# Kernel tuning notes

Measured on AMD Instinct MI355X. Metric: run time of the kernel, lower is better.

Reference implementation:

```python
import jax, jax.numpy as jnp
import numpy as np


def setup_inputs() -> dict:
    key = jax.random.key(0)
    ks = jax.random.split(key, 8)
    B, CAST, H, IN = 2048, 128, 256, 256
    return {
        "x": jax.random.normal(ks[0], (B, IN), dtype=jnp.float32),
        "batch_idxs": jnp.arange(B, dtype=jnp.int64),
        "actor_ids": jax.random.randint(ks[1], (B,), 0, CAST).astype(jnp.int64),
        "story_stop_idxs": jax.random.randint(ks[2], (128,), 0, B).astype(jnp.int64),
        "state": jax.random.normal(ks[3], (B, CAST, H), dtype=jnp.float32),
        "w_ih": jax.random.normal(ks[4], (3 * H, IN), dtype=jnp.float32) * 0.05,
        "w_hh": jax.random.normal(ks[5], (3 * H, H), dtype=jnp.float32) * 0.05,
        "b_ih": jax.random.normal(ks[6], (3 * H,), dtype=jnp.float32) * 0.05,
        "b_hh": jax.random.normal(ks[7], (3 * H,), dtype=jnp.float32) * 0.05,
    }


def _gru_cell(x, h, w_ih, w_hh, b_ih, b_hh):
    # torch.nn.GRUCell math
    H = h.shape[-1]
    gi = x @ w_ih.T + b_ih  # [n, 3H]
    gh = h @ w_hh.T + b_hh  # [n, 3H]
    i_r, i_z, i_n = gi[:, :H], gi[:, H:2 * H], gi[:, 2 * H:]
    h_r, h_z, h_n = gh[:, :H], gh[:, H:2 * H], gh[:, 2 * H:]
    r = jax.nn.sigmoid(i_r + h_r)
    z = jax.nn.sigmoid(i_z + h_z)
    n = jnp.tanh(i_n + r * h_n)
    return (1.0 - z) * n + z * h


def reference(x, batch_idxs, actor_ids, story_stop_idxs, state, w_ih, w_hh, b_ih, b_hh):
    cast_size = state.shape[1]
    actor_ids = jnp.clip(actor_ids, 0, cast_size - 1)
    aid = actor_ids[batch_idxs]  # convert_idxs: actor slot per active story
    # gather indexed actor states
    selected = state[batch_idxs, aid]  # [n_active, H]
    # GRU-cell update
    new_selected = _gru_cell(x, selected, w_ih, w_hh, b_ih, b_hh)
    # scatter back into persistent memory
    new_state = state.at[batch_idxs, aid].set(new_selected)
    # zero out finished stories
    new_state = new_state.at[story_stop_idxs].set(0.0)
    return new_selected, new_state
```

## Files before the change

kernel.cpp:

```cpp
#include <hip/hip_runtime.h>

#define B_TOTAL 2048
#define CAST    128
#define HDIM    256
#define INDIM   256
#define BM      8
#define GRU_BLOCKS (B_TOTAL / BM)
#define ROW_F4     (CAST * HDIM / 4)

typedef float fx4 __attribute__((ext_vector_type(4)));

__global__ __launch_bounds__(256) void k_init(int* rowaid, int* rowstop) {
    int t = blockIdx.x * blockDim.x + threadIdx.x;
    if (t < B_TOTAL) { rowaid[t] = -1; rowstop[t] = 0; }
}

__global__ __launch_bounds__(256) void k_prep(
    const int* __restrict__ batch_idxs, const int* __restrict__ actor_ids,
    const int* __restrict__ story_stop, int n_stop,
    const float* __restrict__ w_ih, const float* __restrict__ w_hh,
    int* rowaid, int* rowstop, float* wtI, float* wtH) {
    const int h = threadIdx.x;
    if (blockIdx.x < 8) {
        int t = blockIdx.x * 256 + h;
        int row = batch_idxs[t];
        int a = actor_ids[row];
        a = a < 0 ? 0 : (a > CAST - 1 ? CAST - 1 : a);
        rowaid[row] = a;
        if (t < n_stop) rowstop[story_stop[t]] = 1;
    } else {
        int id  = blockIdx.x - 8;
        int mat = id / 192;
        int rem = id % 192;
        int g   = rem / 64;
        int k4  = rem % 64;
        const float* w = mat ? w_hh : w_ih;
        float*      wt = mat ? wtH  : wtI;
        float4 wv = *(const float4*)(w + ((size_t)(g * HDIM + h) * INDIM + k4 * 4));
        *(float4*)(wt + ((size_t)((k4 * 3 + g) * HDIM + h)) * 4) = wv;
    }
}

__global__ __launch_bounds__(256) void k_main(
    const float* __restrict__ x, const int* __restrict__ batch_idxs,
    const int* __restrict__ actor_ids, const float* __restrict__ state,
    const float* __restrict__ wtI, const float* __restrict__ wtH,
    const float* __restrict__ b_ih, const float* __restrict__ b_hh,
    const int* __restrict__ rowaid, const int* __restrict__ rowstop,
    float* __restrict__ out_sel, float* __restrict__ out_state) {
    __shared__ float xs[BM][INDIM];
    __shared__ float ss[BM][HDIM];
    const int h = threadIdx.x;

    if (blockIdx.x < GRU_BLOCKS) {
        const int b0 = blockIdx.x * BM;
        #pragma unroll
        for (int r = 0; r < BM; ++r) {
            int g  = b0 + r;
            int bi = batch_idxs[g];
            int a  = actor_ids[bi];
            a = a < 0 ? 0 : (a > CAST - 1 ? CAST - 1 : a);
            xs[r][h] = x[(size_t)g * INDIM + h];
            ss[r][h] = state[((size_t)bi * CAST + a) * HDIM + h];
        }
        __syncthreads();

        float air[BM], aiz[BM], ain[BM], ahr[BM], ahz[BM], ahn[BM];
        #pragma unroll
        for (int r = 0; r < BM; ++r) { air[r]=0.f; aiz[r]=0.f; ain[r]=0.f; ahr[r]=0.f; ahz[r]=0.f; ahn[r]=0.f; }

        const float4* __restrict__ wtI4 = (const float4*)wtI;
        const float4* __restrict__ wtH4 = (const float4*)wtH;

        for (int k4 = 0; k4 < INDIM / 4; ++k4) {
            float4 wir = wtI4[(k4 * 3 + 0) * HDIM + h];
            float4 wiz = wtI4[(k4 * 3 + 1) * HDIM + h];
            float4 win = wtI4[(k4 * 3 + 2) * HDIM + h];
            float4 whr = wtH4[(k4 * 3 + 0) * HDIM + h];
            float4 whz = wtH4[(k4 * 3 + 1) * HDIM + h];
            float4 whn = wtH4[(k4 * 3 + 2) * HDIM + h];
            #pragma unroll
            for (int r = 0; r < BM; ++r) {
                float4 xv = *(const float4*)(&xs[r][k4 * 4]);
                float4 sv = *(const float4*)(&ss[r][k4 * 4]);
                air[r] = fmaf(xv.w, wir.w, fmaf(xv.z, wir.z, fmaf(xv.y, wir.y, fmaf(xv.x, wir.x, air[r]))));
                aiz[r] = fmaf(xv.w, wiz.w, fmaf(xv.z, wiz.z, fmaf(xv.y, wiz.y, fmaf(xv.x, wiz.x, aiz[r]))));
                ain[r] = fmaf(xv.w, win.w, fmaf(xv.z, win.z, fmaf(xv.y, win.y, fmaf(xv.x, win.x, ain[r]))));
                ahr[r] = fmaf(sv.w, whr.w, fmaf(sv.z, whr.z, fmaf(sv.y, whr.y, fmaf(sv.x, whr.x, ahr[r]))));
                ahz[r] = fmaf(sv.w, whz.w, fmaf(sv.z, whz.z, fmaf(sv.y, whz.y, fmaf(sv.x, whz.x, ahz[r]))));
                ahn[r] = fmaf(sv.w, whn.w, fmaf(sv.z, whn.z, fmaf(sv.y, whn.y, fmaf(sv.x, whn.x, ahn[r]))));
            }
        }

        const float bir = b_ih[h], biz = b_ih[HDIM + h], bin = b_ih[2 * HDIM + h];
        const float bhr = b_hh[h], bhz = b_hh[HDIM + h], bhn = b_hh[2 * HDIM + h];

        #pragma unroll
        for (int r = 0; r < BM; ++r) {
            int g  = b0 + r;
            int bi = batch_idxs[g];
            int a  = actor_ids[bi];
            a = a < 0 ? 0 : (a > CAST - 1 ? CAST - 1 : a);
            float ir = air[r] + bir, iz = aiz[r] + biz, inn = ain[r] + bin;
            float hr = ahr[r] + bhr, hz = ahz[r] + bhz, hn = ahn[r] + bhn;
            float rr = 1.f / (1.f + __expf(-(ir + hr)));
            float zz = 1.f / (1.f + __expf(-(iz + hz)));
            float nn = tanhf(inn + rr * hn);
            float val = (1.f - zz) * nn + zz * ss[r][h];
            out_sel[(size_t)g * HDIM + h] = val;
            if (!rowstop[bi]) out_state[((size_t)bi * CAST + a) * HDIM + h] = val;
        }
    } else {
        const int  b = blockIdx.x - GRU_BLOCKS;
        const int  t = threadIdx.x;
        const long base = (long)b * ROW_F4;
        const fx4* __restrict__ src = (const fx4*)state + base + t;
        fx4* __restrict__ dst = (fx4*)out_state + base + t;

        if (rowstop[b]) {
            const fx4 z = (fx4)(0.f);
            #pragma unroll
            for (int j = 0; j < ROW_F4 / 256; ++j)
                __builtin_nontemporal_store(z, dst + j * 256);
            return;
        }

        const int aid = __builtin_amdgcn_readfirstlane(rowaid[b]);
        const int w   = __builtin_amdgcn_readfirstlane(t >> 6);
        const int jskip = ((aid & 3) == w) ? (aid >> 2) : -1;

        #pragma unroll
        for (int g2 = 0; g2 < 2; ++g2) {
            fx4 d[16];
            #pragma unroll
            for (int i = 0; i < 16; ++i)
                d[i] = __builtin_nontemporal_load(src + (g2 * 16 + i) * 256);
            #pragma unroll
            for (int i = 0; i < 16; ++i) {
                if (g2 * 16 + i != jskip)
                    __builtin_nontemporal_store(d[i], dst + (g2 * 16 + i) * 256);
            }
        }
    }
}

extern "C" void kernel_launch(void* const* d_in, const int* in_sizes, int n_in,
                              void* d_out, int out_size, void* d_ws, size_t ws_size,
                              hipStream_t stream) {
    const float* x          = (const float*)d_in[0];
    const int*   batch_idxs = (const int*)d_in[1];
    const int*   actor_ids  = (const int*)d_in[2];
    const int*   story_stop = (const int*)d_in[3];
    const float* state      = (const float*)d_in[4];
    const float* w_ih       = (const float*)d_in[5];
    const float* w_hh       = (const float*)d_in[6];
    const float* b_ih       = (const float*)d_in[7];
    const float* b_hh       = (const float*)d_in[8];
    const int    n_stop     = in_sizes[3];

    float* out_sel   = (float*)d_out;
    float* out_state = out_sel + (size_t)B_TOTAL * HDIM;

    int*   rowaid  = (int*)d_ws;
    int*   rowstop = rowaid + B_TOTAL;
    float* wtI     = (float*)((char*)d_ws + 16384);
    float* wtH     = wtI + (size_t)3 * HDIM * INDIM;

    k_init<<<(B_TOTAL + 255) / 256, 256, 0, stream>>>(rowaid, rowstop);
    k_prep<<<8 + 384, 256, 0, stream>>>(batch_idxs, actor_ids, story_stop, n_stop,
                                        w_ih, w_hh, rowaid, rowstop, wtI, wtH);
    k_main<<<GRU_BLOCKS + B_TOTAL, 256, 0, stream>>>(
        x, batch_idxs, actor_ids, state, wtI, wtH, b_ih, b_hh,
        rowaid, rowstop, out_sel, out_state);
}
```

Before: 159.8 us.

## Move bulk state copy into prep kernel and scatter GRU results afterward

The full state copy now runs in the prep kernel as a grid-strided, coalesced copy alongside the weight transpose. The GRU kernel then overwrites the selected rows and zeroes the stopped rows, so the copy no longer needs per-row actor-skip logic or the rowaid table. The init kernel becomes a memset. In exchange the copy writes every selected slot and the GRU kernel writes them again. The zeroing blocks and the GRU writes also run concurrently, and correctness depends on the rowstop check preventing a race on the same rows.

```diff
diff --git a/kernel.cpp b/kernel.cpp
--- a/kernel.cpp
+++ b/kernel.cpp
@@ -7,140 +7,127 @@
 #define BM      8
 #define GRU_BLOCKS (B_TOTAL / BM)
 #define ROW_F4     (CAST * HDIM / 4)
+#define COPY_BLOCKS 2048
+#define N4_TOTAL   ((long)B_TOTAL * CAST * HDIM / 4)
 
 typedef float fx4 __attribute__((ext_vector_type(4)));
 
-__global__ __launch_bounds__(256) void k_init(int* rowaid, int* rowstop) {
-    int t = blockIdx.x * blockDim.x + threadIdx.x;
-    if (t < B_TOTAL) { rowaid[t] = -1; rowstop[t] = 0; }
-}
-
-__global__ __launch_bounds__(256) void k_prep(
-    const int* __restrict__ batch_idxs, const int* __restrict__ actor_ids,
+__global__ __launch_bounds__(256) void k_copyprep(
+    const float* __restrict__ state, float* __restrict__ out_state,
     const int* __restrict__ story_stop, int n_stop,
     const float* __restrict__ w_ih, const float* __restrict__ w_hh,
-    int* rowaid, int* rowstop, float* wtI, float* wtH) {
-    const int h = threadIdx.x;
-    if (blockIdx.x < 8) {
-        int t = blockIdx.x * 256 + h;
-        int row = batch_idxs[t];
-        int a = actor_ids[row];
-        a = a < 0 ? 0 : (a > CAST - 1 ? CAST - 1 : a);
-        rowaid[row] = a;
+    int* rowstop, float* wtI, float* wtH) {
+    const int t = threadIdx.x;
+    if (blockIdx.x < COPY_BLOCKS) {
+        const long stride = (long)COPY_BLOCKS * 256;
+        const long base = (long)blockIdx.x * 256 + t;
+        const fx4* __restrict__ src = (const fx4*)state;
+        fx4* __restrict__ dst = (fx4*)out_state;
+        #pragma unroll
+        for (int g = 0; g < 4; ++g) {
+            fx4 d[8];
+            #pragma unroll
+            for (int i = 0; i < 8; ++i)
+                d[i] = src[base + (long)(g * 8 + i) * stride];
+            #pragma unroll
+            for (int i = 0; i < 8; ++i)
+                __builtin_nontemporal_store(d[i], &dst[base + (long)(g * 8 + i) * stride]);
+        }
+    } else if (blockIdx.x == COPY_BLOCKS) {
         if (t < n_stop) rowstop[story_stop[t]] = 1;
     } else {
-        int id  = blockIdx.x - 8;
+        int id  = blockIdx.x - (COPY_BLOCKS + 1);
         int mat = id / 192;
         int rem = id % 192;
         int g   = rem / 64;
         int k4  = rem % 64;
         const float* w = mat ? w_hh : w_ih;
         float*      wt = mat ? wtH  : wtI;
-        float4 wv = *(const float4*)(w + ((size_t)(g * HDIM + h) * INDIM + k4 * 4));
-        *(float4*)(wt + ((size_t)((k4 * 3 + g) * HDIM + h)) * 4) = wv;
+        float4 wv = *(const float4*)(w + ((size_t)(g * HDIM + t) * INDIM + k4 * 4));
+        *(float4*)(wt + ((size_t)((k4 * 3 + g) * HDIM + t)) * 4) = wv;
     }
 }
 
-__global__ __launch_bounds__(256) void k_main(
+__global__ __launch_bounds__(256) void k_gru(
     const float* __restrict__ x, const int* __restrict__ batch_idxs,
     const int* __restrict__ actor_ids, const float* __restrict__ state,
     const float* __restrict__ wtI, const float* __restrict__ wtH,
     const float* __restrict__ b_ih, const float* __restrict__ b_hh,
-    const int* __restrict__ rowaid, const int* __restrict__ rowstop,
-    float* __restrict__ out_sel, float* __restrict__ out_state) {
+    const int* __restrict__ rowstop, const int* __restrict__ story_stop,
+    int n_stop, float* __restrict__ out_sel, float* __restrict__ out_state) {
     __shared__ float xs[BM][INDIM];
     __shared__ float ss[BM][HDIM];
     const int h = threadIdx.x;
 
-    if (blockIdx.x < GRU_BLOCKS) {
-        const int b0 = blockIdx.x * BM;
-        #pragma unroll
-        for (int r = 0; r < BM; ++r) {
-            int g  = b0 + r;
-            int bi = batch_idxs[g];
-            int a  = actor_ids[bi];
-            a = a < 0 ? 0 : (a > CAST - 1 ? CAST - 1 : a);
-            xs[r][h] = x[(size_t)g * INDIM + h];
-            ss[r][h] = state[((size_t)bi * CAST + a) * HDIM + h];
-        }
-        __syncthreads();
-
-        float air[BM], aiz[BM], ain[BM], ahr[BM], ahz[BM], ahn[BM];
-        #pragma unroll
-        for (int r = 0; r < BM; ++r) { air[r]=0.f; aiz[r]=0.f; ain[r]=0.f; ahr[r]=0.f; ahz[r]=0.f; ahn[r]=0.f; }
-
-        const float4* __restrict__ wtI4 = (const float4*)wtI;
-        const float4* __restrict__ wtH4 = (const float4*)wtH;
-
-        for (int k4 = 0; k4 < INDIM / 4; ++k4) {
-            float4 wir = wtI4[(k4 * 3 + 0) * HDIM + h];
-            float4 wiz = wtI4[(k4 * 3 + 1) * HDIM + h];
-            float4 win = wtI4[(k4 * 3 + 2) * HDIM + h];
-            float4 whr = wtH4[(k4 * 3 + 0) * HDIM + h];
-            float4 whz = wtH4[(k4 * 3 + 1) * HDIM + h];
-            float4 whn = wtH4[(k4 * 3 + 2) * HDIM + h];
-            #pragma unroll
-            for (int r = 0; r < BM; ++r) {
-                float4 xv = *(const float4*)(&xs[r][k4 * 4]);
-                float4 sv = *(const float4*)(&ss[r][k4 * 4]);
-                air[r] = fmaf(xv.w, wir.w, fmaf(xv.z, wir.z, fmaf(xv.y, wir.y, fmaf(xv.x, wir.x, air[r]))));
-                aiz[r] = fmaf(xv.w, wiz.w, fmaf(xv.z, wiz.z, fmaf(xv.y, wiz.y, fmaf(xv.x, wiz.x, aiz[r]))));
-                ain[r] = fmaf(xv.w, win.w, fmaf(xv.z, win.z, fmaf(xv.y, win.y, fmaf(xv.x, win.x, ain[r]))));
-                ahr[r] = fmaf(sv.w, whr.w, fmaf(sv.z, whr.z, fmaf(sv.y, whr.y, fmaf(sv.x, whr.x, ahr[r]))));
-                ahz[r] = fmaf(sv.w, whz.w, fmaf(sv.z, whz.z, fmaf(sv.y, whz.y, fmaf(sv.x, whz.x, ahz[r]))));
-                ahn[r] = fmaf(sv.w, whn.w, fmaf(sv.z, whn.z, fmaf(sv.y, whn.y, fmaf(sv.x, whn.x, ahn[r]))));
-            }
-        }
-
-        const float bir = b_ih[h], biz = b_ih[HDIM + h], bin = b_ih[2 * HDIM + h];
-        const float bhr = b_hh[h], bhz = b_hh[HDIM + h], bhn = b_hh[2 * HDIM + h];
-
-        #pragma unroll
-        for (int r = 0; r < BM; ++r) {
-            int g  = b0 + r;
-            int bi = batch_idxs[g];
-            int a  = actor_ids[bi];
-            a = a < 0 ? 0 : (a > CAST - 1 ? CAST - 1 : a);
-            float ir = air[r] + bir, iz = aiz[r] + biz, inn = ain[r] + bin;
-            float hr = ahr[r] + bhr, hz = ahz[r] + bhz, hn = ahn[r] + bhn;
-            float rr = 1.f / (1.f + __expf(-(ir + hr)));
-            float zz = 1.f / (1.f + __expf(-(iz + hz)));
-            float nn = tanhf(inn + rr * hn);
-            float val = (1.f - zz) * nn + zz * ss[r][h];
-            out_sel[(size_t)g * HDIM + h] = val;
-            if (!rowstop[bi]) out_state[((size_t)bi * CAST + a) * HDIM + h] = val;
-        }
-    } else {
-        const int  b = blockIdx.x - GRU_BLOCKS;
-        const int  t = threadIdx.x;
-        const long base = (long)b * ROW_F4;
-        const fx4* __restrict__ src = (const fx4*)state + base + t;
-        fx4* __restrict__ dst = (fx4*)out_state + base + t;
-
-        if (rowstop[b]) {
+    if (blockIdx.x >= GRU_BLOCKS) {
+        int zb = blockIdx.x - GRU_BLOCKS;
+        if (zb < n_stop) {
+            long base = (long)story_stop[zb] * ROW_F4;
+            fx4* __restrict__ dst = (fx4*)out_state + base + h;
             const fx4 z = (fx4)(0.f);
             #pragma unroll
             for (int j = 0; j < ROW_F4 / 256; ++j)
                 __builtin_nontemporal_store(z, dst + j * 256);
-            return;
         }
+        return;
+    }
 
-        const int aid = __builtin_amdgcn_readfirstlane(rowaid[b]);
-        const int w   = __builtin_amdgcn_readfirstlane(t >> 6);
-        const int jskip = ((aid & 3) == w) ? (aid >> 2) : -1;
+    const int b0 = blockIdx.x * BM;
+    #pragma unroll
+    for (int r = 0; r < BM; ++r) {
+        int g  = b0 + r;
+        int bi = batch_idxs[g];
+        int a  = actor_ids[bi];
+        a = a < 0 ? 0 : (a > CAST - 1 ? CAST - 1 : a);
+        xs[r][h] = x[(size_t)g * INDIM + h];
+        ss[r][h] = state[((size_t)bi * CAST + a) * HDIM + h];
+    }
+    __syncthreads();
 
+    float air[BM], aiz[BM], ain[BM], ahr[BM], ahz[BM], ahn[BM];
+    #pragma unroll
+    for (int r = 0; r < BM; ++r) { air[r]=0.f; aiz[r]=0.f; ain[r]=0.f; ahr[r]=0.f; ahz[r]=0.f; ahn[r]=0.f; }
+
+    const float4* __restrict__ wtI4 = (const float4*)wtI;
+    const float4* __restrict__ wtH4 = (const float4*)wtH;
+
+    for (int k4 = 0; k4 < INDIM / 4; ++k4) {
+        float4 wir = wtI4[(k4 * 3 + 0) * HDIM + h];
+        float4 wiz = wtI4[(k4 * 3 + 1) * HDIM + h];
+        float4 win = wtI4[(k4 * 3 + 2) * HDIM + h];
+        float4 whr = wtH4[(k4 * 3 + 0) * HDIM + h];
+        float4 whz = wtH4[(k4 * 3 + 1) * HDIM + h];
+        float4 whn = wtH4[(k4 * 3 + 2) * HDIM + h];
         #pragma unroll
-        for (int g2 = 0; g2 < 2; ++g2) {
-            fx4 d[16];
-            #pragma unroll
-            for (int i = 0; i < 16; ++i)
-                d[i] = __builtin_nontemporal_load(src + (g2 * 16 + i) * 256);
-            #pragma unroll
-            for (int i = 0; i < 16; ++i) {
-                if (g2 * 16 + i != jskip)
-                    __builtin_nontemporal_store(d[i], dst + (g2 * 16 + i) * 256);
-            }
+        for (int r = 0; r < BM; ++r) {
+            float4 xv = *(const float4*)(&xs[r][k4 * 4]);
+            float4 sv = *(const float4*)(&ss[r][k4 * 4]);
+            air[r] = fmaf(xv.w, wir.w, fmaf(xv.z, wir.z, fmaf(xv.y, wir.y, fmaf(xv.x, wir.x, air[r]))));
+            aiz[r] = fmaf(xv.w, wiz.w, fmaf(xv.z, wiz.z, fmaf(xv.y, wiz.y, fmaf(xv.x, wiz.x, aiz[r]))));
+            ain[r] = fmaf(xv.w, win.w, fmaf(xv.z, win.z, fmaf(xv.y, win.y, fmaf(xv.x, win.x, ain[r]))));
+            ahr[r] = fmaf(sv.w, whr.w, fmaf(sv.z, whr.z, fmaf(sv.y, whr.y, fmaf(sv.x, whr.x, ahr[r]))));
+            ahz[r] = fmaf(sv.w, whz.w, fmaf(sv.z, whz.z, fmaf(sv.y, whz.y, fmaf(sv.x, whz.x, ahz[r]))));
+            ahn[r] = fmaf(sv.w, whn.w, fmaf(sv.z, whn.z, fmaf(sv.y, whn.y, fmaf(sv.x, whn.x, ahn[r]))));
         }
+    }
+
+    const float bir = b_ih[h], biz = b_ih[HDIM + h], bin = b_ih[2 * HDIM + h];
+    const float bhr = b_hh[h], bhz = b_hh[HDIM + h], bhn = b_hh[2 * HDIM + h];
+
+    #pragma unroll
+    for (int r = 0; r < BM; ++r) {
+        int g  = b0 + r;
+        int bi = batch_idxs[g];
+        int a  = actor_ids[bi];
+        a = a < 0 ? 0 : (a > CAST - 1 ? CAST - 1 : a);
+        float ir = air[r] + bir, iz = aiz[r] + biz, inn = ain[r] + bin;
+        float hr = ahr[r] + bhr, hz = ahz[r] + bhz, hn = ahn[r] + bhn;
+        float rr = 1.f / (1.f + __expf(-(ir + hr)));
+        float zz = 1.f / (1.f + __expf(-(iz + hz)));
+        float nn = tanhf(inn + rr * hn);
+        float val = (1.f - zz) * nn + zz * ss[r][h];
+        out_sel[(size_t)g * HDIM + h] = val;
+        if (!rowstop[bi]) out_state[((size_t)bi * CAST + a) * HDIM + h] = val;
     }
 }
 
@@ -161,15 +148,14 @@
     float* out_sel   = (float*)d_out;
     float* out_state = out_sel + (size_t)B_TOTAL * HDIM;
 
-    int*   rowaid  = (int*)d_ws;
-    int*   rowstop = rowaid + B_TOTAL;
+    int*   rowstop = (int*)d_ws;
     float* wtI     = (float*)((char*)d_ws + 16384);
     float* wtH     = wtI + (size_t)3 * HDIM * INDIM;
 
-    k_init<<<(B_TOTAL + 255) / 256, 256, 0, stream>>>(rowaid, rowstop);
-    k_prep<<<8 + 384, 256, 0, stream>>>(batch_idxs, actor_ids, story_stop, n_stop,
-                                        w_ih, w_hh, rowaid, rowstop, wtI, wtH);
-    k_main<<<GRU_BLOCKS + B_TOTAL, 256, 0, stream>>>(
+    hipMemsetAsync(rowstop, 0, B_TOTAL * sizeof(int), stream);
+    k_copyprep<<<COPY_BLOCKS + 1 + 384, 256, 0, stream>>>(
+        state, out_state, story_stop, n_stop, w_ih, w_hh, rowstop, wtI, wtH);
+    k_gru<<<GRU_BLOCKS + 128, 256, 0, stream>>>(
         x, batch_idxs, actor_ids, state, wtI, wtH, b_ih, b_hh,
-        rowaid, rowstop, out_sel, out_state);
+        rowstop, story_stop, n_stop, out_sel, out_state);
 }
```

Result: slower. 200.2 us (+25.3%).

## Stream state copy through LDS with global_load_lds and reorder copy/GRU blocks

Applied to the files above, without the earlier changes.

The bulk state copy now issues direct global-to-LDS loads in batches of eight 16-byte loads, then reads back from LDS and stores to global. Each wave now owns a contiguous quarter of a row instead of striding across it. Copy blocks are scheduled before the GRU blocks, and the init kernel is replaced by two hipMemsetAsync calls. The aim is higher copy bandwidth and less launch overhead. In exchange, shared memory per block rises to 32 KB, which can lower occupancy, and the copy drops its nontemporal hints, waits on vmcnt(0) every batch, and keeps fewer loads in flight per thread.

```diff
diff --git a/kernel.cpp b/kernel.cpp
--- a/kernel.cpp
+++ b/kernel.cpp
@@ -5,14 +5,16 @@
 #define HDIM    256
 #define INDIM   256
 #define BM      8
-#define GRU_BLOCKS (B_TOTAL / BM)
-#define ROW_F4     (CAST * HDIM / 4)
+#define GRU_BLOCKS  (B_TOTAL / BM)
+#define COPY_BLOCKS B_TOTAL
+#define ROW_FLOATS  (CAST * HDIM)
 
 typedef float fx4 __attribute__((ext_vector_type(4)));
 
-__global__ __launch_bounds__(256) void k_init(int* rowaid, int* rowstop) {
-    int t = blockIdx.x * blockDim.x + threadIdx.x;
-    if (t < B_TOTAL) { rowaid[t] = -1; rowstop[t] = 0; }
+__device__ __forceinline__ void gld_lds16(const float* g, float* l) {
+    __builtin_amdgcn_global_load_lds(
+        (const __attribute__((address_space(1))) void*)g,
+        (__attribute__((address_space(3))) void*)l, 16, 0, 0);
 }
 
 __global__ __launch_bounds__(256) void k_prep(
@@ -20,14 +22,14 @@
     const int* __restrict__ story_stop, int n_stop,
     const float* __restrict__ w_ih, const float* __restrict__ w_hh,
     int* rowaid, int* rowstop, float* wtI, float* wtH) {
-    const int h = threadIdx.x;
+    const int t = threadIdx.x;
     if (blockIdx.x < 8) {
-        int t = blockIdx.x * 256 + h;
-        int row = batch_idxs[t];
+        int g = blockIdx.x * 256 + t;
+        int row = batch_idxs[g];
         int a = actor_ids[row];
         a = a < 0 ? 0 : (a > CAST - 1 ? CAST - 1 : a);
         rowaid[row] = a;
-        if (t < n_stop) rowstop[story_stop[t]] = 1;
+        if (g < n_stop) rowstop[story_stop[g]] = 1;
     } else {
         int id  = blockIdx.x - 8;
         int mat = id / 192;
@@ -36,8 +38,8 @@
         int k4  = rem % 64;
         const float* w = mat ? w_hh : w_ih;
         float*      wt = mat ? wtH  : wtI;
-        float4 wv = *(const float4*)(w + ((size_t)(g * HDIM + h) * INDIM + k4 * 4));
-        *(float4*)(wt + ((size_t)((k4 * 3 + g) * HDIM + h)) * 4) = wv;
+        float4 wv = *(const float4*)(w + ((size_t)(g * HDIM + t) * INDIM + k4 * 4));
+        *(float4*)(wt + ((size_t)((k4 * 3 + g) * HDIM + t)) * 4) = wv;
     }
 }
 
@@ -48,99 +50,107 @@
     const float* __restrict__ b_ih, const float* __restrict__ b_hh,
     const int* __restrict__ rowaid, const int* __restrict__ rowstop,
     float* __restrict__ out_sel, float* __restrict__ out_state) {
-    __shared__ float xs[BM][INDIM];
-    __shared__ float ss[BM][HDIM];
+    __shared__ float smem[8192];
     const int h = threadIdx.x;
 
-    if (blockIdx.x < GRU_BLOCKS) {
-        const int b0 = blockIdx.x * BM;
-        #pragma unroll
-        for (int r = 0; r < BM; ++r) {
-            int g  = b0 + r;
-            int bi = batch_idxs[g];
-            int a  = actor_ids[bi];
-            a = a < 0 ? 0 : (a > CAST - 1 ? CAST - 1 : a);
-            xs[r][h] = x[(size_t)g * INDIM + h];
-            ss[r][h] = state[((size_t)bi * CAST + a) * HDIM + h];
-        }
-        __syncthreads();
-
-        float air[BM], aiz[BM], ain[BM], ahr[BM], ahz[BM], ahn[BM];
-        #pragma unroll
-        for (int r = 0; r < BM; ++r) { air[r]=0.f; aiz[r]=0.f; ain[r]=0.f; ahr[r]=0.f; ahz[r]=0.f; ahn[r]=0.f; }
-
-        const float4* __restrict__ wtI4 = (const float4*)wtI;
-        const float4* __restrict__ wtH4 = (const float4*)wtH;
-
-        for (int k4 = 0; k4 < INDIM / 4; ++k4) {
-            float4 wir = wtI4[(k4 * 3 + 0) * HDIM + h];
-            float4 wiz = wtI4[(k4 * 3 + 1) * HDIM + h];
-            float4 win = wtI4[(k4 * 3 + 2) * HDIM + h];
-            float4 whr = wtH4[(k4 * 3 + 0) * HDIM + h];
-            float4 whz = wtH4[(k4 * 3 + 1) * HDIM + h];
-            float4 whn = wtH4[(k4 * 3 + 2) * HDIM + h];
-            #pragma unroll
-            for (int r = 0; r < BM; ++r) {
-                float4 xv = *(const float4*)(&xs[r][k4 * 4]);
-                float4 sv = *(const float4*)(&ss[r][k4 * 4]);
-                air[r] = fmaf(xv.w, wir.w, fmaf(xv.z, wir.z, fmaf(xv.y, wir.y, fmaf(xv.x, wir.x, air[r]))));
-                aiz[r] = fmaf(xv.w, wiz.w, fmaf(xv.z, wiz.z, fmaf(xv.y, wiz.y, fmaf(xv.x, wiz.x, aiz[r]))));
-                ain[r] = fmaf(xv.w, win.w, fmaf(xv.z, win.z, fmaf(xv.y, win.y, fmaf(xv.x, win.x, ain[r]))));
-                ahr[r] = fmaf(sv.w, whr.w, fmaf(sv.z, whr.z, fmaf(sv.y, whr.y, fmaf(sv.x, whr.x, ahr[r]))));
-                ahz[r] = fmaf(sv.w, whz.w, fmaf(sv.z, whz.z, fmaf(sv.y, whz.y, fmaf(sv.x, whz.x, ahz[r]))));
-                ahn[r] = fmaf(sv.w, whn.w, fmaf(sv.z, whn.z, fmaf(sv.y, whn.y, fmaf(sv.x, whn.x, ahn[r]))));
-            }
-        }
-
-        const float bir = b_ih[h], biz = b_ih[HDIM + h], bin = b_ih[2 * HDIM + h];
-        const float bhr = b_hh[h], bhz = b_hh[HDIM + h], bhn = b_hh[2 * HDIM + h];
-
-        #pragma unroll
-        for (int r = 0; r < BM; ++r) {
-            int g  = b0 + r;
-            int bi = batch_idxs[g];
-            int a  = actor_ids[bi];
-            a = a < 0 ? 0 : (a > CAST - 1 ? CAST - 1 : a);
-            float ir = air[r] + bir, iz = aiz[r] + biz, inn = ain[r] + bin;
-            float hr = ahr[r] + bhr, hz = ahz[r] + bhz, hn = ahn[r] + bhn;
-            float rr = 1.f / (1.f + __expf(-(ir + hr)));
-            float zz = 1.f / (1.f + __expf(-(iz + hz)));
-            float nn = tanhf(inn + rr * hn);
-            float val = (1.f - zz) * nn + zz * ss[r][h];
-            out_sel[(size_t)g * HDIM + h] = val;
-            if (!rowstop[bi]) out_state[((size_t)bi * CAST + a) * HDIM + h] = val;
-        }
-    } else {
-        const int  b = blockIdx.x - GRU_BLOCKS;
-        const int  t = threadIdx.x;
-        const long base = (long)b * ROW_F4;
-        const fx4* __restrict__ src = (const fx4*)state + base + t;
-        fx4* __restrict__ dst = (fx4*)out_state + base + t;
+    if (blockIdx.x < COPY_BLOCKS) {
+        const int  b    = blockIdx.x;
+        const int  w    = h >> 6;
+        const int  lane = h & 63;
+        const long qbase = (long)b * ROW_FLOATS + (long)w * 8192;
+        float* __restrict__ dst = out_state + qbase + lane * 4;
 
         if (rowstop[b]) {
             const fx4 z = (fx4)(0.f);
             #pragma unroll
-            for (int j = 0; j < ROW_F4 / 256; ++j)
-                __builtin_nontemporal_store(z, dst + j * 256);
+            for (int op = 0; op < 32; ++op)
+                __builtin_nontemporal_store(z, (fx4*)(dst + op * 256));
             return;
         }
 
+        const float* __restrict__ src = state + qbase + lane * 4;
+        float* lw = smem + w * 2048;
         const int aid = __builtin_amdgcn_readfirstlane(rowaid[b]);
-        const int w   = __builtin_amdgcn_readfirstlane(t >> 6);
-        const int jskip = ((aid & 3) == w) ? (aid >> 2) : -1;
+        const int sk  = aid - w * 32;
 
         #pragma unroll
-        for (int g2 = 0; g2 < 2; ++g2) {
-            fx4 d[16];
+        for (int bt = 0; bt < 4; ++bt) {
             #pragma unroll
-            for (int i = 0; i < 16; ++i)
-                d[i] = __builtin_nontemporal_load(src + (g2 * 16 + i) * 256);
+            for (int k = 0; k < 8; ++k)
+                gld_lds16(src + (bt * 8 + k) * 256, lw + k * 256);
+            asm volatile("s_waitcnt vmcnt(0)" ::: "memory");
+            __builtin_amdgcn_sched_barrier(0);
             #pragma unroll
-            for (int i = 0; i < 16; ++i) {
-                if (g2 * 16 + i != jskip)
-                    __builtin_nontemporal_store(d[i], dst + (g2 * 16 + i) * 256);
+            for (int k = 0; k < 8; ++k) {
+                const int op = bt * 8 + k;
+                if (op != sk) {
+                    fx4 v = *(const fx4*)(lw + k * 256 + lane * 4);
+                    *(fx4*)(dst + op * 256) = v;
+                }
             }
         }
+        return;
+    }
+
+    float (*xs)[INDIM] = (float(*)[INDIM])smem;
+    float (*ss)[HDIM]  = (float(*)[HDIM])(smem + BM * INDIM);
+    const int b0 = (blockIdx.x - COPY_BLOCKS) * BM;
+
+    #pragma unroll
+    for (int r = 0; r < BM; ++r) {
+        int g  = b0 + r;
+        int bi = batch_idxs[g];
+        int a  = actor_ids[bi];
+        a = a < 0 ? 0 : (a > CAST - 1 ? CAST - 1 : a);
+        xs[r][h] = x[(size_t)g * INDIM + h];
+        ss[r][h] = state[((size_t)bi * CAST + a) * HDIM + h];
+    }
+    __syncthreads();
+
+    float air[BM], aiz[BM], ain[BM], ahr[BM], ahz[BM], ahn[BM];
+    #pragma unroll
+    for (int r = 0; r < BM; ++r) { air[r]=0.f; aiz[r]=0.f; ain[r]=0.f; ahr[r]=0.f; ahz[r]=0.f; ahn[r]=0.f; }
+
+    const float4* __restrict__ wtI4 = (const float4*)wtI;
+    const float4* __restrict__ wtH4 = (const float4*)wtH;
+
+    for (int k4 = 0; k4 < INDIM / 4; ++k4) {
+        float4 wir = wtI4[(k4 * 3 + 0) * HDIM + h];
+        float4 wiz = wtI4[(k4 * 3 + 1) * HDIM + h];
+        float4 win = wtI4[(k4 * 3 + 2) * HDIM + h];
+        float4 whr = wtH4[(k4 * 3 + 0) * HDIM + h];
+        float4 whz = wtH4[(k4 * 3 + 1) * HDIM + h];
+        float4 whn = wtH4[(k4 * 3 + 2) * HDIM + h];
+        #pragma unroll
+        for (int r = 0; r < BM; ++r) {
+            float4 xv = *(const float4*)(&xs[r][k4 * 4]);
+            float4 sv = *(const float4*)(&ss[r][k4 * 4]);
+            air[r] = fmaf(xv.w, wir.w, fmaf(xv.z, wir.z, fmaf(xv.y, wir.y, fmaf(xv.x, wir.x, air[r]))));
+            aiz[r] = fmaf(xv.w, wiz.w, fmaf(xv.z, wiz.z, fmaf(xv.y, wiz.y, fmaf(xv.x, wiz.x, aiz[r]))));
+            ain[r] = fmaf(xv.w, win.w, fmaf(xv.z, win.z, fmaf(xv.y, win.y, fmaf(xv.x, win.x, ain[r]))));
+            ahr[r] = fmaf(sv.w, whr.w, fmaf(sv.z, whr.z, fmaf(sv.y, whr.y, fmaf(sv.x, whr.x, ahr[r]))));
+            ahz[r] = fmaf(sv.w, whz.w, fmaf(sv.z, whz.z, fmaf(sv.y, whz.y, fmaf(sv.x, whz.x, ahz[r]))));
+            ahn[r] = fmaf(sv.w, whn.w, fmaf(sv.z, whn.z, fmaf(sv.y, whn.y, fmaf(sv.x, whn.x, ahn[r]))));
+        }
+    }
+
+    const float bir = b_ih[h], biz = b_ih[HDIM + h], bin = b_ih[2 * HDIM + h];
+    const float bhr = b_hh[h], bhz = b_hh[HDIM + h], bhn = b_hh[2 * HDIM + h];
+
+    #pragma unroll
+    for (int r = 0; r < BM; ++r) {
+        int g  = b0 + r;
+        int bi = batch_idxs[g];
+        int a  = actor_ids[bi];
+        a = a < 0 ? 0 : (a > CAST - 1 ? CAST - 1 : a);
+        float ir = air[r] + bir, iz = aiz[r] + biz, inn = ain[r] + bin;
+        float hr = ahr[r] + bhr, hz = ahz[r] + bhz, hn = ahn[r] + bhn;
+        float rr = 1.f / (1.f + __expf(-(ir + hr)));
+        float zz = 1.f / (1.f + __expf(-(iz + hz)));
+        float nn = tanhf(inn + rr * hn);
+        float val = (1.f - zz) * nn + zz * ss[r][h];
+        out_sel[(size_t)g * HDIM + h] = val;
+        if (!rowstop[bi]) out_state[((size_t)bi * CAST + a) * HDIM + h] = val;
     }
 }
 
@@ -166,10 +176,11 @@
     float* wtI     = (float*)((char*)d_ws + 16384);
     float* wtH     = wtI + (size_t)3 * HDIM * INDIM;
 
-    k_init<<<(B_TOTAL + 255) / 256, 256, 0, stream>>>(rowaid, rowstop);
+    hipMemsetAsync(rowaid, 0xFF, B_TOTAL * sizeof(int), stream);
+    hipMemsetAsync(rowstop, 0, B_TOTAL * sizeof(int), stream);
     k_prep<<<8 + 384, 256, 0, stream>>>(batch_idxs, actor_ids, story_stop, n_stop,
                                         w_ih, w_hh, rowaid, rowstop, wtI, wtH);
-    k_main<<<GRU_BLOCKS + B_TOTAL, 256, 0, stream>>>(
+    k_main<<<COPY_BLOCKS + GRU_BLOCKS, 256, 0, stream>>>(
         x, batch_idxs, actor_ids, state, wtI, wtH, b_ih, b_hh,
         rowaid, rowstop, out_sel, out_state);
 }
```

Result: slower. 216.8 us (+35.7%).
